# Optimization experiments

Hardware: AMD Instinct MI355X
Metric: run time of the kernel (lower is better)

The kernel has to match this reference:

```python
import jax, jax.numpy as jnp
import numpy as np

N, E, D, L, R, G, NRXN = 100000, 400000, 256, 3, 4, 2000, 10


def setup_inputs() -> dict:
    key = jax.random.key(0)
    ks = jax.random.split(key, 12)
    s = 1.0 / np.sqrt(D).astype(np.float32)
    return {
        "node_feature": jax.random.normal(ks[0], (N, D), jnp.float32),
        "flag_W": jax.random.normal(ks[1], (2, D), jnp.float32) * s,
        "flag_b": jax.random.normal(ks[2], (D,), jnp.float32) * s,
        "W_self": jax.random.normal(ks[3], (L, D, D), jnp.float32) * s,
        "b_self": jax.random.normal(ks[4], (L, D), jnp.float32) * s,
        "W_rel": jax.random.normal(ks[5], (L, R, D, D), jnp.float32) * s,
        "edge_src": jax.random.randint(ks[6], (E,), 0, N, jnp.int32),
        "edge_dst": jax.random.randint(ks[7], (E,), 0, N, jnp.int32),
        "edge_type": jax.random.randint(ks[8], (E,), 0, R, jnp.int32),
        "batch": jnp.sort(jax.random.randint(ks[9], (N,), 0, G, jnp.int32)),
        "reaction": jax.random.randint(ks[10], (G,), 0, NRXN, jnp.int32),
        "center_mask": jax.random.randint(ks[11], (N,), 0, 2, jnp.int32).astype(bool),
    }


def _rgcn_layer(x, Wself, bself, Wrel, edge_src, edge_dst, edge_type, deg):
    # Relation-wise transform on all nodes [R, N, D], then per-edge gather by
    # (edge_type, src). Masks over edge_type partition edges, so overwriting
    # messages[mask] per relation == selecting the relation's transform per edge.
    h = jnp.einsum('nd,rde->rne', x, Wrel)
    messages = h[edge_type, edge_src]                         # [E, D]
    agg = jax.ops.segment_sum(messages, edge_dst, num_segments=x.shape[0]) / deg
    return jax.nn.relu(x @ Wself + bself + agg)


def reference(node_feature, flag_W, flag_b, W_self, b_self, W_rel,
              edge_src, edge_dst, edge_type, batch, reaction, center_mask):
    n = node_feature.shape[0]
    # flags = [zeros, center_mask]; node_input = node_feature + flag_linear(flags)
    flags = jnp.stack([jnp.zeros((n,), jnp.float32),
                       center_mask.astype(jnp.float32)], axis=-1)  # [N, 2]
    x = node_feature + flags @ flag_W + flag_b
    # degree normalization over destinations (same every layer), clamp min 1
    deg = jnp.maximum(
        jax.ops.segment_sum(jnp.ones((edge_dst.shape[0],), jnp.float32),
                            edge_dst, num_segments=n), 1.0)[:, None]
    hiddens = []
    for l in range(L):
        x = _rgcn_layer(x, W_self[l], b_self[l], W_rel[l],
                        edge_src, edge_dst, edge_type, deg)
        hiddens.append(x)
    node_enc = jnp.concatenate(hiddens, axis=-1)              # [N, L*D]
    # segment mean over graphs
    gsum = jax.ops.segment_sum(node_enc, batch, num_segments=G)
    gcnt = jnp.maximum(
        jax.ops.segment_sum(jnp.ones((n,), jnp.float32), batch, num_segments=G),
        1.0)[:, None]
    graph_feature = gsum / gcnt                               # [G, L*D]
    rxn = jax.nn.one_hot(reaction, NRXN, dtype=jnp.float32)   # [G, NRXN]
    graph_context = jnp.concatenate([graph_feature, rxn], axis=-1)
    node_context = jnp.concatenate(
        [node_enc, node_feature, graph_context[batch]], axis=-1)  # [N, 1802]
    return node_context, graph_context
```

## Files before the change

kernel.cpp:

```cpp
#include <hip/hip_runtime.h>
#include <hip/hip_bf16.h>

typedef _Float16 f16x8 __attribute__((ext_vector_type(8)));
typedef float f32x4 __attribute__((ext_vector_type(4)));

namespace {
constexpr int N_ = 100000;
constexpr int E_ = 400000;
constexpr int D_ = 256;
constexpr int L_ = 3;
constexpr int R_ = 4;
constexpr int G_ = 2000;
constexpr int NRXN_ = 10;
constexpr int CTXW = L_*D_ + D_ + L_*D_ + NRXN_;
constexpr int GCTXW = L_*D_ + NRXN_;
constexpr int NKT = (R_+1)*D_/32;
constexpr int NR = N_*R_;
constexpr int NB2 = (NR + 2047)/2048;
}


__global__ void k_zero(int* __restrict__ p, int n) {
  int i = blockIdx.x*256 + threadIdx.x;
  if (i < n) p[i] = 0;
}

__global__ void k_detect(const unsigned char* __restrict__ cm, int* __restrict__ meta) {
  int tid = threadIdx.x;
  int ok_i = 1, ok_f = 1;
  for (int i = tid; i < 4096; i += 256) {
    unsigned b = cm[i];
    int m = i & 3;
    if (m == 0)      { if (b > 1) ok_i = 0; if (b != 0) ok_f = 0; }
    else if (m == 1) { if (b) { ok_i = 0; ok_f = 0; } }
    else if (m == 2) { if (b) ok_i = 0; if (b != 0 && b != 0x80) ok_f = 0; }
    else             { if (b) ok_i = 0; if (b != 0 && b != 0x3f) ok_f = 0; }
  }
  int all_i = __syncthreads_and(ok_i);
  int all_f = __syncthreads_and(ok_f);
  if (tid == 0) meta[0] = all_i ? 0 : (all_f ? 1 : 2);
}

__global__ void k_hist2(const int* __restrict__ dst, const int* __restrict__ typ,
                        int* __restrict__ hist, int n) {
  int i = blockIdx.x*256 + threadIdx.x;
  if (i < n) atomicAdd(&hist[dst[i]*4 + typ[i]], 1);
}

__global__ void k_hist(const int* __restrict__ key, int* __restrict__ hist, int n) {
  int i = blockIdx.x*256 + threadIdx.x;
  if (i < n) atomicAdd(&hist[key[i]], 1);
}

__global__ void k_scan1(const int* __restrict__ h, int* __restrict__ out,
                        int* __restrict__ bsum, int n) {
  __shared__ int sh[256];
  int t = threadIdx.x;
  int base = blockIdx.x*2048 + t*8;
  int v[8]; int s = 0;
  #pragma unroll
  for (int j = 0; j < 8; ++j) { v[j] = (base+j < n) ? h[base+j] : 0; s += v[j]; }
  sh[t] = s; __syncthreads();
  for (int off = 1; off < 256; off <<= 1) {
    int x = (t >= off) ? sh[t-off] : 0;
    __syncthreads();
    sh[t] += x;
    __syncthreads();
  }
  int ex = sh[t] - s;
  #pragma unroll
  for (int j = 0; j < 8; ++j) { if (base+j < n) out[base+j] = ex; ex += v[j]; }
  if (t == 255) bsum[blockIdx.x] = sh[255];
}

__global__ void k_scan2(int* __restrict__ b, int nb) {
  __shared__ int sh[256];
  int t = threadIdx.x;
  int s = (t < nb) ? b[t] : 0;
  sh[t] = s; __syncthreads();
  for (int off = 1; off < 256; off <<= 1) {
    int x = (t >= off) ? sh[t-off] : 0;
    __syncthreads();
    sh[t] += x;
    __syncthreads();
  }
  if (t < nb) b[t] = sh[t] - s;
}

__global__ void k_scan3(int* __restrict__ eoff, const int* __restrict__ bsum,
                        int* __restrict__ cursor, int n, int total) {
  int i = blockIdx.x*256 + threadIdx.x;
  if (i < n) {
    int v = eoff[i] + bsum[i >> 11];
    eoff[i] = v;
    cursor[i] = v;
  }
  if (i == 0) eoff[n] = total;
}

__global__ void k_scatter2(const int* __restrict__ src, const int* __restrict__ dst,
                           const int* __restrict__ typ, int* __restrict__ cursor,
                           int* __restrict__ out, int n) {
  int i = blockIdx.x*256 + threadIdx.x;
  if (i < n) {
    int key = dst[i]*4 + typ[i];
    int p = atomicAdd(&cursor[key], 1);
    out[p] = src[i];
  }
}

__global__ void k_scan_small(const int* __restrict__ gh, int* __restrict__ goff, int g) {
  __shared__ int sh[256];
  int t = threadIdx.x;
  int v[8]; int s = 0;
  #pragma unroll
  for (int j = 0; j < 8; ++j) { int idx = t*8+j; v[j] = (idx < g) ? gh[idx] : 0; s += v[j]; }
  sh[t] = s; __syncthreads();
  for (int off = 1; off < 256; off <<= 1) {
    int x = (t >= off) ? sh[t-off] : 0;
    __syncthreads();
    sh[t] += x;
    __syncthreads();
  }
  int ex = sh[t] - s;
  #pragma unroll
  for (int j = 0; j < 8; ++j) { int idx = t*8+j; if (idx < g) goff[idx] = ex; ex += v[j]; }
  if (t == 255) goff[g] = sh[255];
}

__global__ void k_pack_w(const float* __restrict__ Wrel, const float* __restrict__ Wself,
                         f16x8* __restrict__ Bp) {
  int id = blockIdx.x*256 + threadIdx.x;
  if (id >= L_*NKT*16*64) return;
  int lane = id & 63; int rest = id >> 6;
  int ct = rest & 15; rest >>= 4;
  int kt = rest % NKT; int l = rest / NKT;
  int q = lane >> 4, ln = lane & 15;
  int col = ct*16 + ln;
  f16x8 o;
  #pragma unroll
  for (int j = 0; j < 8; ++j) {
    int k = kt*32 + q*8 + j;
    float v = (k < R_*D_) ? Wrel[((size_t)l*R_*D_ + k)*D_ + col]
                          : Wself[((size_t)l*D_ + (k - R_*D_))*D_ + col];
    o[j] = (_Float16)v;
  }
  Bp[id] = o;
}

__global__ void k_node_init(const float* __restrict__ nf, const float* __restrict__ fW,
                            const float* __restrict__ fb, const void* __restrict__ cm,
                            const int* __restrict__ meta, _Float16* __restrict__ xa,
                            float* __restrict__ out) {
  int n = blockIdx.x, c = threadIdx.x;
  float v = nf[(size_t)n*D_ + c];
  out[(size_t)n*CTXW + 768 + c] = v;
  int mode = meta[0];
  bool mk;
  if (mode == 0)      mk = ((const int*)cm)[n] != 0;
  else if (mode == 1) mk = ((const float*)cm)[n] != 0.f;
  else                mk = ((const unsigned char*)cm)[n] != 0;
  float x0 = v + (mk ? fW[D_ + c] : 0.f) + fb[c];
  xa[(size_t)n*D_ + c] = (_Float16)x0;
}

__global__ __launch_bounds__(256, 4)
void k_layer(const _Float16* __restrict__ xin, const f16x8* __restrict__ Bp,
             const float* __restrict__ bias, const int* __restrict__ eoff2,
             const int* __restrict__ es, float* __restrict__ outp,
             _Float16* __restrict__ xout) {
  __shared__ f16x8 As16[2][32*32];
  const int tid = threadIdx.x;
  const int lane = tid & 63, wave = tid >> 6;
  const int q = lane >> 4, ln = lane & 15;
  const int m0 = blockIdx.x * 32;
  const int kch = lane & 7;
  const int row = wave*8 + (lane >> 3);
  const int nd  = m0 + row;

  int oo[5];
  #pragma unroll
  for (int j = 0; j < 5; ++j) oo[j] = eoff2[nd*4 + j];
  const int degt = oo[4] - oo[0];
  const float invd = 1.0f / (float)(degt > 1 ? degt : 1);

  f32x4 acc[2][4];
  #pragma unroll
  for (int rt = 0; rt < 2; ++rt)
    #pragma unroll
    for (int cc = 0; cc < 4; ++cc)
      acc[rt][cc] = f32x4{0.f,0.f,0.f,0.f};

  {
    const _Float16* r0 = xin + (size_t)(m0 + ln)*D_;
    const _Float16* r1 = xin + (size_t)(m0 + 16 + ln)*D_;
    #pragma unroll
    for (int kt = 0; kt < 8; ++kt) {
      f16x8 a0 = *(const f16x8*)(r0 + kt*32 + q*8);
      f16x8 a1 = *(const f16x8*)(r1 + kt*32 + q*8);
      f16x8 b[4];
      #pragma unroll
      for (int cc = 0; cc < 4; ++cc)
        b[cc] = Bp[(size_t)((32 + kt)*16 + wave*4 + cc)*64 + lane];
      #pragma unroll
      for (int cc = 0; cc < 4; ++cc) {
        acc[0][cc] = __builtin_amdgcn_mfma_f32_16x16x32_f16(a0, b[cc], acc[0][cc], 0,0,0);
        acc[1][cc] = __builtin_amdgcn_mfma_f32_16x16x32_f16(a1, b[cc], acc[1][cc], 0,0,0);
      }
    }
  }

  #pragma unroll
  for (int r = 0; r < R_; ++r) {
    f32x4 ax[8];
    #pragma unroll
    for (int i = 0; i < 8; ++i) ax[i] = f32x4{0.f,0.f,0.f,0.f};
    for (int e = oo[r]; e < oo[r+1]; ++e) {
      int src = es[e];
      const f16x8* sp = (const f16x8*)(xin + (size_t)src*D_);
      f16x8 w0 = sp[0*8 + kch];
      f16x8 w1 = sp[1*8 + kch];
      f16x8 w2 = sp[2*8 + kch];
      f16x8 w3 = sp[3*8 + kch];
      ax[0] += f32x4{(float)w0[0],(float)w0[1],(float)w0[2],(float)w0[3]};
      ax[1] += f32x4{(float)w0[4],(float)w0[5],(float)w0[6],(float)w0[7]};
      ax[2] += f32x4{(float)w1[0],(float)w1[1],(float)w1[2],(float)w1[3]};
      ax[3] += f32x4{(float)w1[4],(float)w1[5],(float)w1[6],(float)w1[7]};
      ax[4] += f32x4{(float)w2[0],(float)w2[1],(float)w2[2],(float)w2[3]};
      ax[5] += f32x4{(float)w2[4],(float)w2[5],(float)w2[6],(float)w2[7]};
      ax[6] += f32x4{(float)w3[0],(float)w3[1],(float)w3[2],(float)w3[3]};
      ax[7] += f32x4{(float)w3[4],(float)w3[5],(float)w3[6],(float)w3[7]};
    }
    f16x8* dstb = &As16[r & 1][row*32];
    #pragma unroll
    for (int i = 0; i < 4; ++i) {
      f32x4 lo = ax[2*i], hi = ax[2*i+1];
      f16x8 o;
      o[0] = (_Float16)(lo[0]*invd); o[1] = (_Float16)(lo[1]*invd);
      o[2] = (_Float16)(lo[2]*invd); o[3] = (_Float16)(lo[3]*invd);
      o[4] = (_Float16)(hi[0]*invd); o[5] = (_Float16)(hi[1]*invd);
      o[6] = (_Float16)(hi[2]*invd); o[7] = (_Float16)(hi[3]*invd);
      dstb[(i*8 + kch) ^ (row & 7)] = o;
    }
    __syncthreads();
    const f16x8* As = As16[r & 1];
    #pragma unroll
    for (int kt = 0; kt < 8; ++kt) {
      f16x8 a0 = As[(size_t)ln*32      + ((kt*4 + q) ^ (ln & 7))];
      f16x8 a1 = As[(size_t)(16+ln)*32 + ((kt*4 + q) ^ (ln & 7))];
      f16x8 b[4];
      #pragma unroll
      for (int cc = 0; cc < 4; ++cc)
        b[cc] = Bp[(size_t)((r*8 + kt)*16 + wave*4 + cc)*64 + lane];
      #pragma unroll
      for (int cc = 0; cc < 4; ++cc) {
        acc[0][cc] = __builtin_amdgcn_mfma_f32_16x16x32_f16(a0, b[cc], acc[0][cc], 0,0,0);
        acc[1][cc] = __builtin_amdgcn_mfma_f32_16x16x32_f16(a1, b[cc], acc[1][cc], 0,0,0);
      }
    }
  }

  #pragma unroll
  for (int cc = 0; cc < 4; ++cc) {
    int col = (wave*4 + cc)*16 + ln;
    float bv = bias[col];
    #pragma unroll
    for (int rt = 0; rt < 2; ++rt) {
      #pragma unroll
      for (int i = 0; i < 4; ++i) {
        int rrow = m0 + rt*16 + q*4 + i;
        float v = acc[rt][cc][i] + bv;
        v = fmaxf(v, 0.f);
        outp[(size_t)rrow*CTXW + col] = v;
        if (xout) xout[(size_t)rrow*D_ + col] = (_Float16)v;
      }
    }
  }
}

__global__ void k_pool(float* __restrict__ out, const int* __restrict__ goff,
                       const int* __restrict__ rxn) {
  int g = blockIdx.x, t = threadIdx.x;
  int s = goff[g], e = goff[g+1];
  int cnt = e - s;
  float inv = 1.0f / (float)(cnt > 1 ? cnt : 1);
  float a0 = 0.f, a1 = 0.f, a2 = 0.f;
  for (int nn = s; nn < e; ++nn) {
    size_t base = (size_t)nn*CTXW;
    a0 += out[base + t];
    a1 += out[base + 256 + t];
    a2 += out[base + 512 + t];
  }
  a0 *= inv; a1 *= inv; a2 *= inv;
  float rx = 0.f;
  int rv = rxn[g];
  size_t gbase = (size_t)N_*CTXW + (size_t)g*GCTXW;
  out[gbase + t]       = a0;
  out[gbase + 256 + t] = a1;
  out[gbase + 512 + t] = a2;
  if (t < NRXN_) { rx = (rv == t) ? 1.f : 0.f; out[gbase + 768 + t] = rx; }
  for (int nn = s; nn < e; ++nn) {
    size_t nb = (size_t)nn*CTXW + 1024;
    out[nb + t]       = a0;
    out[nb + 256 + t] = a1;
    out[nb + 512 + t] = a2;
    if (t < NRXN_) out[nb + 768 + t] = rx;
  }
}

extern "C" void kernel_launch(void* const* d_in, const int* in_sizes, int n_in,
                              void* d_out, int out_size, void* d_ws, size_t ws_size,
                              hipStream_t stream) {
  const float* node_feature = (const float*)d_in[0];
  const float* flag_W  = (const float*)d_in[1];
  const float* flag_b  = (const float*)d_in[2];
  const float* W_self  = (const float*)d_in[3];
  const float* b_self  = (const float*)d_in[4];
  const float* W_rel   = (const float*)d_in[5];
  const int* edge_src  = (const int*)d_in[6];
  const int* edge_dst  = (const int*)d_in[7];
  const int* edge_type = (const int*)d_in[8];
  const int* batch     = (const int*)d_in[9];
  const int* reaction  = (const int*)d_in[10];
  const void* cmask    = d_in[11];
  float* out = (float*)d_out;

  char* ws = (char*)d_ws;
  size_t off = 0;
  auto alloc = [&](size_t bytes) {
    void* p = ws + off;
    off = (off + bytes + 255) & ~(size_t)255;
    return p;
  };
  int* meta          = (int*)alloc(256);
  _Float16* xa       = (_Float16*)alloc((size_t)N_*D_*2);
  _Float16* xb       = (_Float16*)alloc((size_t)N_*D_*2);
  f16x8* Bp          = (f16x8*)alloc((size_t)L_*NKT*16*64*16);
  int* eoff2         = (int*)alloc((size_t)(NR+1)*4);
  int* cursor        = (int*)alloc((size_t)NR*4);
  int* ghist         = (int*)alloc((size_t)G_*4);
  int* goff          = (int*)alloc((size_t)(G_+1)*4);
  int* bsum          = (int*)alloc(1024);
  int* esorted       = (int*)alloc((size_t)E_*4);
  (void)in_sizes; (void)n_in; (void)out_size; (void)ws_size;

  k_detect<<<1, 256, 0, stream>>>((const unsigned char*)cmask, meta);
  k_zero<<<(NR+255)/256, 256, 0, stream>>>(cursor, NR);
  k_zero<<<(G_+255)/256, 256, 0, stream>>>(ghist, G_);
  k_hist2<<<(E_+255)/256, 256, 0, stream>>>(edge_dst, edge_type, cursor, E_);
  k_scan1<<<NB2, 256, 0, stream>>>(cursor, eoff2, bsum, NR);
  k_scan2<<<1, 256, 0, stream>>>(bsum, NB2);
  k_scan3<<<(NR+255)/256, 256, 0, stream>>>(eoff2, bsum, cursor, NR, E_);
  k_scatter2<<<(E_+255)/256, 256, 0, stream>>>(edge_src, edge_dst, edge_type, cursor, esorted, E_);
  k_hist<<<(N_+255)/256, 256, 0, stream>>>(batch, ghist, N_);
  k_scan_small<<<1, 256, 0, stream>>>(ghist, goff, G_);
  k_pack_w<<<(L_*NKT*16*64 + 255)/256, 256, 0, stream>>>(W_rel, W_self, Bp);
  k_node_init<<<N_, 256, 0, stream>>>(node_feature, flag_W, flag_b, cmask, meta, xa, out);

  const int nblk = N_ / 32;
  k_layer<<<nblk, 256, 0, stream>>>(xa, Bp,          b_self,       eoff2, esorted, out,       xb);
  k_layer<<<nblk, 256, 0, stream>>>(xb, Bp + 40960,  b_self + 256, eoff2, esorted, out + 256, xa);
  k_layer<<<nblk, 256, 0, stream>>>(xa, Bp + 81920,  b_self + 512, eoff2, esorted, out + 512, nullptr);

  k_pool<<<G_, 256, 0, stream>>>(out, goff, reaction);
}
```

Measured before the change: 1.511 ms.

## Vectorize init and pool kernels, prefetch B fragments and gathered rows in layer

Node init now handles 8 nodes per block with 128-bit loads and stores, and writes packed f16x8 values. Pooling now uses f32x4 loads and stores on 192 threads, with two accumulators over nodes; separate threads write the reaction one-hot. The layer kernel double-buffers the weight B fragments one k-step ahead and loads the next edge's source row before accumulating the current one, to hide load latency. The risks are higher register pressure under launch_bounds(256,4) and 16-byte accesses on output rows whose 1802-float stride is not 16-byte aligned.

```diff
diff --git a/kernel.cpp b/kernel.cpp
--- a/kernel.cpp
+++ b/kernel.cpp
@@ -152,16 +152,30 @@
                             const float* __restrict__ fb, const void* __restrict__ cm,
                             const int* __restrict__ meta, _Float16* __restrict__ xa,
                             float* __restrict__ out) {
-  int n = blockIdx.x, c = threadIdx.x;
-  float v = nf[(size_t)n*D_ + c];
-  out[(size_t)n*CTXW + 768 + c] = v;
+  int t = threadIdx.x;
+  int n = blockIdx.x*8 + (t >> 5);
+  int c = (t & 31)*8;
+  const f32x4* nf4 = (const f32x4*)(nf + (size_t)n*D_ + c);
+  f32x4 v0 = nf4[0], v1 = nf4[1];
+  float* ob = out + (size_t)n*CTXW + 768 + c;
+  *(f32x4*)ob = v0;
+  *(f32x4*)(ob + 4) = v1;
   int mode = meta[0];
   bool mk;
   if (mode == 0)      mk = ((const int*)cm)[n] != 0;
   else if (mode == 1) mk = ((const float*)cm)[n] != 0.f;
   else                mk = ((const unsigned char*)cm)[n] != 0;
-  float x0 = v + (mk ? fW[D_ + c] : 0.f) + fb[c];
-  xa[(size_t)n*D_ + c] = (_Float16)x0;
+  float m = mk ? 1.f : 0.f;
+  f32x4 w0 = *(const f32x4*)(fW + D_ + c);
+  f32x4 w1 = *(const f32x4*)(fW + D_ + c + 4);
+  f32x4 b0 = *(const f32x4*)(fb + c);
+  f32x4 b1 = *(const f32x4*)(fb + c + 4);
+  f32x4 x0 = v0 + w0*m + b0;
+  f32x4 x1 = v1 + w1*m + b1;
+  f16x8 o;
+  o[0]=(_Float16)x0[0]; o[1]=(_Float16)x0[1]; o[2]=(_Float16)x0[2]; o[3]=(_Float16)x0[3];
+  o[4]=(_Float16)x1[0]; o[5]=(_Float16)x1[1]; o[6]=(_Float16)x1[2]; o[7]=(_Float16)x1[3];
+  *(f16x8*)(xa + (size_t)n*D_ + c) = o;
 }
 
 __global__ __launch_bounds__(256, 4)
@@ -193,19 +207,28 @@
 
   {
     const _Float16* r0 = xin + (size_t)(m0 + ln)*D_;
-    const _Float16* r1 = xin + (size_t)(m0 + 16 + ln)*D_;
+    const _Float16* r1 = r0 + (size_t)16*D_;
+    const f16x8* bb = Bp + ((size_t)(32*16 + wave*4))*64 + lane;
+    f16x8 bc[4];
+    #pragma unroll
+    for (int cc = 0; cc < 4; ++cc) bc[cc] = bb[cc*64];
     #pragma unroll
     for (int kt = 0; kt < 8; ++kt) {
       f16x8 a0 = *(const f16x8*)(r0 + kt*32 + q*8);
       f16x8 a1 = *(const f16x8*)(r1 + kt*32 + q*8);
-      f16x8 b[4];
-      #pragma unroll
-      for (int cc = 0; cc < 4; ++cc)
-        b[cc] = Bp[(size_t)((32 + kt)*16 + wave*4 + cc)*64 + lane];
+      f16x8 bn[4];
+      if (kt < 7) {
+        #pragma unroll
+        for (int cc = 0; cc < 4; ++cc) bn[cc] = bb[(kt+1)*1024 + cc*64];
+      }
       #pragma unroll
       for (int cc = 0; cc < 4; ++cc) {
-        acc[0][cc] = __builtin_amdgcn_mfma_f32_16x16x32_f16(a0, b[cc], acc[0][cc], 0,0,0);
-        acc[1][cc] = __builtin_amdgcn_mfma_f32_16x16x32_f16(a1, b[cc], acc[1][cc], 0,0,0);
+        acc[0][cc] = __builtin_amdgcn_mfma_f32_16x16x32_f16(a0, bc[cc], acc[0][cc], 0,0,0);
+        acc[1][cc] = __builtin_amdgcn_mfma_f32_16x16x32_f16(a1, bc[cc], acc[1][cc], 0,0,0);
+      }
+      if (kt < 7) {
+        #pragma unroll
+        for (int cc = 0; cc < 4; ++cc) bc[cc] = bn[cc];
       }
     }
   }
@@ -215,13 +238,8 @@
     f32x4 ax[8];
     #pragma unroll
     for (int i = 0; i < 8; ++i) ax[i] = f32x4{0.f,0.f,0.f,0.f};
-    for (int e = oo[r]; e < oo[r+1]; ++e) {
-      int src = es[e];
-      const f16x8* sp = (const f16x8*)(xin + (size_t)src*D_);
-      f16x8 w0 = sp[0*8 + kch];
-      f16x8 w1 = sp[1*8 + kch];
-      f16x8 w2 = sp[2*8 + kch];
-      f16x8 w3 = sp[3*8 + kch];
+
+    auto accum = [&](f16x8 w0, f16x8 w1, f16x8 w2, f16x8 w3) {
       ax[0] += f32x4{(float)w0[0],(float)w0[1],(float)w0[2],(float)w0[3]};
       ax[1] += f32x4{(float)w0[4],(float)w0[5],(float)w0[6],(float)w0[7]};
       ax[2] += f32x4{(float)w1[0],(float)w1[1],(float)w1[2],(float)w1[3]};
@@ -230,7 +248,23 @@
       ax[5] += f32x4{(float)w2[4],(float)w2[5],(float)w2[6],(float)w2[7]};
       ax[6] += f32x4{(float)w3[0],(float)w3[1],(float)w3[2],(float)w3[3]};
       ax[7] += f32x4{(float)w3[4],(float)w3[5],(float)w3[6],(float)w3[7]};
-    }
+    };
+
+    {
+      int e0 = oo[r], e1 = oo[r+1];
+      if (e0 < e1) {
+        const f16x8* sp = (const f16x8*)(xin + (size_t)es[e0]*D_);
+        f16x8 w0 = sp[kch], w1 = sp[8+kch], w2 = sp[16+kch], w3 = sp[24+kch];
+        for (int e = e0 + 1; e < e1; ++e) {
+          const f16x8* sn = (const f16x8*)(xin + (size_t)es[e]*D_);
+          f16x8 n0 = sn[kch], n1 = sn[8+kch], n2 = sn[16+kch], n3 = sn[24+kch];
+          accum(w0, w1, w2, w3);
+          w0 = n0; w1 = n1; w2 = n2; w3 = n3;
+        }
+        accum(w0, w1, w2, w3);
+      }
+    }
+
     f16x8* dstb = &As16[r & 1][row*32];
     #pragma unroll
     for (int i = 0; i < 4; ++i) {
@@ -244,18 +278,27 @@
     }
     __syncthreads();
     const f16x8* As = As16[r & 1];
+    const f16x8* bb = Bp + ((size_t)(r*8*16 + wave*4))*64 + lane;
+    f16x8 bc[4];
+    #pragma unroll
+    for (int cc = 0; cc < 4; ++cc) bc[cc] = bb[cc*64];
     #pragma unroll
     for (int kt = 0; kt < 8; ++kt) {
       f16x8 a0 = As[(size_t)ln*32      + ((kt*4 + q) ^ (ln & 7))];
       f16x8 a1 = As[(size_t)(16+ln)*32 + ((kt*4 + q) ^ (ln & 7))];
-      f16x8 b[4];
-      #pragma unroll
-      for (int cc = 0; cc < 4; ++cc)
-        b[cc] = Bp[(size_t)((r*8 + kt)*16 + wave*4 + cc)*64 + lane];
+      f16x8 bn[4];
+      if (kt < 7) {
+        #pragma unroll
+        for (int cc = 0; cc < 4; ++cc) bn[cc] = bb[(kt+1)*1024 + cc*64];
+      }
       #pragma unroll
       for (int cc = 0; cc < 4; ++cc) {
-        acc[0][cc] = __builtin_amdgcn_mfma_f32_16x16x32_f16(a0, b[cc], acc[0][cc], 0,0,0);
-        acc[1][cc] = __builtin_amdgcn_mfma_f32_16x16x32_f16(a1, b[cc], acc[1][cc], 0,0,0);
+        acc[0][cc] = __builtin_amdgcn_mfma_f32_16x16x32_f16(a0, bc[cc], acc[0][cc], 0,0,0);
+        acc[1][cc] = __builtin_amdgcn_mfma_f32_16x16x32_f16(a1, bc[cc], acc[1][cc], 0,0,0);
+      }
+      if (kt < 7) {
+        #pragma unroll
+        for (int cc = 0; cc < 4; ++cc) bc[cc] = bn[cc];
       }
     }
   }
@@ -284,27 +327,28 @@
   int s = goff[g], e = goff[g+1];
   int cnt = e - s;
   float inv = 1.0f / (float)(cnt > 1 ? cnt : 1);
-  float a0 = 0.f, a1 = 0.f, a2 = 0.f;
-  for (int nn = s; nn < e; ++nn) {
-    size_t base = (size_t)nn*CTXW;
-    a0 += out[base + t];
-    a1 += out[base + 256 + t];
-    a2 += out[base + 512 + t];
-  }
-  a0 *= inv; a1 *= inv; a2 *= inv;
-  float rx = 0.f;
-  int rv = rxn[g];
   size_t gbase = (size_t)N_*CTXW + (size_t)g*GCTXW;
-  out[gbase + t]       = a0;
-  out[gbase + 256 + t] = a1;
-  out[gbase + 512 + t] = a2;
-  if (t < NRXN_) { rx = (rv == t) ? 1.f : 0.f; out[gbase + 768 + t] = rx; }
-  for (int nn = s; nn < e; ++nn) {
-    size_t nb = (size_t)nn*CTXW + 1024;
-    out[nb + t]       = a0;
-    out[nb + 256 + t] = a1;
-    out[nb + 512 + t] = a2;
-    if (t < NRXN_) out[nb + 768 + t] = rx;
+  if (t < 192) {
+    int c = t*4;
+    f32x4 a{0.f,0.f,0.f,0.f}, b{0.f,0.f,0.f,0.f};
+    int nn = s;
+    for (; nn + 1 < e; nn += 2) {
+      f32x4 p = *(const f32x4*)(out + (size_t)nn*CTXW + c);
+      f32x4 q2 = *(const f32x4*)(out + (size_t)(nn+1)*CTXW + c);
+      a += p; b += q2;
+    }
+    if (nn < e) a += *(const f32x4*)(out + (size_t)nn*CTXW + c);
+    a += b;
+    a = a * inv;
+    *(f32x4*)(out + gbase + c) = a;
+    for (int nn2 = s; nn2 < e; ++nn2)
+      *(f32x4*)(out + (size_t)nn2*CTXW + 1024 + c) = a;
+  } else if (t < 192 + NRXN_) {
+    int k = t - 192;
+    float rv = (rxn[g] == k) ? 1.f : 0.f;
+    out[gbase + 768 + k] = rv;
+    for (int nn2 = s; nn2 < e; ++nn2)
+      out[(size_t)nn2*CTXW + 1024 + 768 + k] = rv;
   }
 }
 
@@ -355,7 +399,7 @@
   k_hist<<<(N_+255)/256, 256, 0, stream>>>(batch, ghist, N_);
   k_scan_small<<<1, 256, 0, stream>>>(ghist, goff, G_);
   k_pack_w<<<(L_*NKT*16*64 + 255)/256, 256, 0, stream>>>(W_rel, W_self, Bp);
-  k_node_init<<<N_, 256, 0, stream>>>(node_feature, flag_W, flag_b, cmask, meta, xa, out);
+  k_node_init<<<N_/8, 256, 0, stream>>>(node_feature, flag_W, flag_b, cmask, meta, xa, out);
 
   const int nblk = N_ / 32;
   k_layer<<<nblk, 256, 0, stream>>>(xa, Bp,          b_self,       eoff2, esorted, out,       xb);
```

New measurement: 1.448 ms. 1.04x faster.
